# Optimization experiments

Measured on AMD Instinct MI355X. Metric: run time of the kernel, lower is better.

Reference implementation:

```python
import jax, jax.numpy as jnp
import numpy as np

NUM_GRAPHS = 256
EPS = 1e-5
SLOPE = 0.01

def _lrelu(x):
    return jnp.where(x >= 0, x, SLOPE * x)

def _gcn(x, W, b, src, dst, ew, n_nodes):
    # GCNConv(normalize=False): out[dst] = sum_e ew[e] * (x @ W)[src[e]] + b
    h = x @ W
    msg = h[src] * ew[:, None]
    agg = jax.ops.segment_sum(msg, dst, num_segments=n_nodes)
    return agg + b

def _bn(x, g, beta):
    # training-mode BatchNorm1d over node dim, biased variance
    m = jnp.mean(x, axis=0)
    v = jnp.mean((x - m) ** 2, axis=0)
    return (x - m) * jax.lax.rsqrt(v + EPS) * g + beta

def setup_inputs() -> dict:
    key = jax.random.key(0)
    ks = jax.random.split(key, 20)
    N, E, F0 = 20000, 320000, 1280
    dims = [(F0, 640), (640, 512), (512, 256), (256, 256)]
    inp = {
        'x': jax.random.normal(ks[0], (N, F0), dtype=jnp.float32),
        'edge_index': jax.random.randint(ks[1], (2, E), 0, N, dtype=jnp.int64),
        'edge_weigth': jax.random.uniform(ks[2], (E,), dtype=jnp.float32),
        'batch': jnp.sort(jax.random.randint(ks[3], (N,), 0, NUM_GRAPHS, dtype=jnp.int64)),
    }
    for i, (fi, fo) in enumerate(dims, start=1):
        inp[f'W{i}'] = jax.random.normal(ks[3 + i], (fi, fo), dtype=jnp.float32) * (1.0 / np.sqrt(fi))
        inp[f'b{i}'] = jnp.zeros((fo,), dtype=jnp.float32)
        inp[f'g{i}'] = jnp.ones((fo,), dtype=jnp.float32)
        inp[f'be{i}'] = jnp.zeros((fo,), dtype=jnp.float32)
    fdims = [(256, 128), (128, 64), (64, 2)]
    for i, (fi, fo) in enumerate(fdims, start=1):
        inp[f'Wf{i}'] = jax.random.normal(ks[10 + i], (fi, fo), dtype=jnp.float32) * np.sqrt(2.0 / (fi + fo))
        inp[f'bf{i}'] = jnp.zeros((fo,), dtype=jnp.float32)
    return inp

def reference(x, edge_index, edge_weigth, batch,
              W1, b1, g1, be1, W2, b2, g2, be2,
              W3, b3, g3, be3, W4, b4, g4, be4,
              Wf1, bf1, Wf2, bf2, Wf3, bf3):
    n = x.shape[0]
    src, dst = edge_index[0], edge_index[1]
    h = _lrelu(_bn(_gcn(x, W1, b1, src, dst, edge_weigth, n), g1, be1))
    h = _lrelu(_bn(_gcn(h, W2, b2, src, dst, edge_weigth, n), g2, be2))
    h = _lrelu(_bn(_gcn(h, W3, b3, src, dst, edge_weigth, n), g3, be3))
    h = _lrelu(_bn(_gcn(h, W4, b4, src, dst, edge_weigth, n), g4, be4))
    pooled = jax.ops.segment_sum(h, batch, num_segments=NUM_GRAPHS)  # [G, 256]
    out = _lrelu(pooled @ Wf1 + bf1)
    out = _lrelu(out @ Wf2 + bf2)
    out = _lrelu(out @ Wf3 + bf3)
    return out
```

## Files before the change

kernel.cpp:

```cpp
#include <hip/hip_runtime.h>

typedef short bf16x8 __attribute__((ext_vector_type(8)));
typedef float f32x4  __attribute__((ext_vector_type(4)));

__device__ __forceinline__ float bf2f(unsigned short h){
  union { unsigned int u; float f; } c; c.u = ((unsigned int)h) << 16; return c.f;
}
__device__ __forceinline__ unsigned short f2bf(float f){
  union { float f; unsigned int u; } c; c.f = f;
  unsigned int u = c.u;
  return (unsigned short)((u + 0x7fffu + ((u >> 16) & 1u)) >> 16);
}
__device__ __forceinline__ void gload_lds16(const void* g, void* l){
  __builtin_amdgcn_global_load_lds((const __attribute__((address_space(1))) unsigned int*)g,
                                   (__attribute__((address_space(3))) unsigned int*)l, 16, 0, 0);
}
__device__ __forceinline__ float lrelu(float x){ return x >= 0.f ? x : 0.01f * x; }

__global__ void cvt_f32_bf16(const float* __restrict__ x, unsigned short* __restrict__ o, int n4){
  int i = blockIdx.x * 256 + threadIdx.x;
  if (i >= n4) return;
  float4 v = ((const float4*)x)[i];
  ushort4 r; r.x = f2bf(v.x); r.y = f2bf(v.y); r.z = f2bf(v.z); r.w = f2bf(v.w);
  ((ushort4*)o)[i] = r;
}

__global__ void wt_kernel(const float* __restrict__ Wm, unsigned short* __restrict__ Wt, int K, int Nf){
  __shared__ float tile[32][33];
  int n0 = blockIdx.x * 32, k0 = blockIdx.y * 32;
  int tx = threadIdx.x, ty = threadIdx.y;
  for (int i = ty; i < 32; i += 8)
    tile[i][tx] = Wm[(size_t)(k0 + i) * Nf + n0 + tx];
  __syncthreads();
  for (int i = ty; i < 32; i += 8)
    Wt[(size_t)(n0 + i) * K + k0 + tx] = f2bf(tile[tx][i]);
}

__global__ void hist_kernel(const int* __restrict__ dst, int* __restrict__ hist, int E){
  int e = blockIdx.x * 256 + threadIdx.x;
  if (e < E) atomicAdd(&hist[dst[e]], 1);
}

__global__ void scan_kernel(int* __restrict__ hist, int* __restrict__ cursor, int n, int total){
  __shared__ int partials[1024];
  const int CH = 20;
  int t = threadIdx.x;
  int base = t * CH;
  int local[CH];
  int s = 0;
  for (int i = 0; i < CH; i++){
    int idx = base + i;
    int v = (idx < n) ? hist[idx] : 0;
    local[i] = s; s += v;
  }
  partials[t] = s;
  __syncthreads();
  for (int off = 1; off < 1024; off <<= 1){
    int v = (t >= off) ? partials[t - off] : 0;
    __syncthreads();
    if (t >= off) partials[t] += v;
    __syncthreads();
  }
  int pre = (t == 0) ? 0 : partials[t - 1];
  for (int i = 0; i < CH; i++){
    int idx = base + i;
    if (idx < n){ int v = pre + local[i]; hist[idx] = v; cursor[idx] = v; }
  }
  if (t == 0){ hist[n] = total; }
}

__global__ void scatter_kernel(const int* __restrict__ src, const int* __restrict__ dst,
                               const float* __restrict__ ew, int* __restrict__ cursor,
                               int* __restrict__ so, float* __restrict__ eo, int E){
  int e = blockIdx.x * 256 + threadIdx.x;
  if (e >= E) return;
  int d = dst[e];
  int p = atomicAdd(&cursor[d], 1);
  so[p] = src[e]; eo[p] = ew[e];
}

__global__ __launch_bounds__(256) void gemm_bf16(const unsigned short* __restrict__ A,
                                                 const unsigned short* __restrict__ Bt,
                                                 unsigned short* __restrict__ C,
                                                 int Nf, int K){
  __shared__ unsigned short lsA[128 * 64];
  __shared__ unsigned short lsB[128 * 64];
  const int tid = threadIdx.x;
  const int wave = tid >> 6, lane = tid & 63;
  const int wr = wave >> 1, wc = wave & 1;
  const size_t tm = (size_t)blockIdx.x * 128, tn = (size_t)blockIdx.y * 128;

  f32x4 acc[4][4] = {};

  const int lrow = lane >> 3;
  const int lcol = (lane & 7) * 8;
  const unsigned short* Ab = A  + (tm + wave * 32 + lrow) * (size_t)K + lcol;
  const unsigned short* Bb = Bt + (tn + wave * 32 + lrow) * (size_t)K + lcol;
  unsigned short* lA0 = &lsA[(wave * 32) * 64];
  unsigned short* lB0 = &lsB[(wave * 32) * 64];

  for (int k0 = 0; k0 < K; k0 += 64){
    #pragma unroll
    for (int s = 0; s < 4; s++){
      gload_lds16(Ab + (size_t)s * 8 * K + k0, lA0 + s * 8 * 64);
      gload_lds16(Bb + (size_t)s * 8 * K + k0, lB0 + s * 8 * 64);
    }
    __syncthreads();
    #pragma unroll
    for (int kk = 0; kk < 2; kk++){
      bf16x8 af[4], bfr[4];
      #pragma unroll
      for (int m = 0; m < 4; m++)
        af[m] = *(const bf16x8*)&lsA[(wr * 64 + m * 16 + (lane & 15)) * 64 + kk * 32 + (lane >> 4) * 8];
      #pragma unroll
      for (int n = 0; n < 4; n++)
        bfr[n] = *(const bf16x8*)&lsB[(wc * 64 + n * 16 + (lane & 15)) * 64 + kk * 32 + (lane >> 4) * 8];
      #pragma unroll
      for (int m = 0; m < 4; m++)
        #pragma unroll
        for (int n = 0; n < 4; n++)
          acc[m][n] = __builtin_amdgcn_mfma_f32_16x16x32_bf16(af[m], bfr[n], acc[m][n], 0, 0, 0);
    }
    __syncthreads();
  }
  #pragma unroll
  for (int m = 0; m < 4; m++)
    #pragma unroll
    for (int n = 0; n < 4; n++)
      #pragma unroll
      for (int j = 0; j < 4; j++){
        size_t row = tm + wr * 64 + m * 16 + (lane >> 4) * 4 + j;
        size_t col = tn + wc * 64 + n * 16 + (lane & 15);
        C[row * Nf + col] = f2bf(acc[m][n][j]);
      }
}

template<int F, int G>
__global__ __launch_bounds__((F / 8) * G)
void agg_csr_v(const unsigned short* __restrict__ H,
               const int* __restrict__ rp,
               const int* __restrict__ srcs,
               const float* __restrict__ ews,
               float* __restrict__ AGG){
  constexpr int CH = F / 8;
  const int node = blockIdx.x;
  const int t = threadIdx.x;
  const int c = t % CH, g = t / CH;
  const int e0 = rp[node], e1 = rp[node + 1];
  const size_t coff = (size_t)c * 8;

  float acc[8] = {0.f,0.f,0.f,0.f,0.f,0.f,0.f,0.f};
  int e = e0 + g;
  for (; e + G < e1; e += 2 * G){
    int s0 = srcs[e];     float w0 = ews[e];
    int s1 = srcs[e + G]; float w1 = ews[e + G];
    bf16x8 v0 = *(const bf16x8*)&H[(size_t)s0 * F + coff];
    bf16x8 v1 = *(const bf16x8*)&H[(size_t)s1 * F + coff];
    #pragma unroll
    for (int j = 0; j < 8; j++) acc[j] += w0 * bf2f((unsigned short)v0[j]);
    #pragma unroll
    for (int j = 0; j < 8; j++) acc[j] += w1 * bf2f((unsigned short)v1[j]);
  }
  if (e < e1){
    int s0 = srcs[e]; float w0 = ews[e];
    bf16x8 v0 = *(const bf16x8*)&H[(size_t)s0 * F + coff];
    #pragma unroll
    for (int j = 0; j < 8; j++) acc[j] += w0 * bf2f((unsigned short)v0[j]);
  }

  __shared__ float red[G][F];
  if (g > 0){
    #pragma unroll
    for (int j = 0; j < 8; j++) red[g][c * 8 + j] = acc[j];
  }
  __syncthreads();
  if (g == 0){
    #pragma unroll
    for (int gg = 1; gg < G; gg++)
      #pragma unroll
      for (int j = 0; j < 8; j++) acc[j] += red[gg][c * 8 + j];
    float* orow = AGG + (size_t)node * F + coff;
    #pragma unroll
    for (int j = 0; j < 8; j++) orow[j] = acc[j];
  }
}

__global__ void stats_kernel(const float* __restrict__ AGG, float* __restrict__ sum,
                             float* __restrict__ sumsq, int F){
  int f = blockIdx.x * 256 + threadIdx.x;
  if (f >= F) return;
  int r0 = blockIdx.y * 500;
  const float* p = AGG + (size_t)r0 * F + f;
  float s = 0.f, q = 0.f;
  for (int r = 0; r < 500; r++){ float v = p[(size_t)r * F]; s += v; q += v * v; }
  atomicAdd(&sum[f], s); atomicAdd(&sumsq[f], q);
}

__global__ void norm_kernel(const float* __restrict__ AGG, const float* __restrict__ sum,
                            const float* __restrict__ sumsq, const float* __restrict__ gw,
                            const float* __restrict__ bw, unsigned short* __restrict__ OUT, int F){
  int r = blockIdx.x;
  const float inv = 1.0f / 20000.0f;
  for (int f = threadIdx.x; f < F; f += 256){
    float m = sum[f] * inv;
    float v = fmaxf(sumsq[f] * inv - m * m, 0.f);
    float rs = rsqrtf(v + 1e-5f);
    float x = (AGG[(size_t)r * F + f] - m) * rs * gw[f] + bw[f];
    OUT[(size_t)r * F + f] = f2bf(lrelu(x));
  }
}

__global__ void bounds_kernel(const int* __restrict__ batch, int* __restrict__ gstart, int n){
  int g = threadIdx.x;
  if (g > 256) return;
  int lo = 0, hi = n;
  while (lo < hi){ int mid = (lo + hi) >> 1; if (batch[mid] < g) lo = mid + 1; else hi = mid; }
  gstart[g] = lo;
}

__global__ __launch_bounds__(256) void pool_kernel_v(const unsigned short* __restrict__ A1,
                                                     const int* __restrict__ gstart,
                                                     float* __restrict__ pooled){
  int gph = blockIdx.x;
  int t = threadIdx.x;
  int c = t & 31, g = t >> 5;
  int r0 = gstart[gph], r1 = gstart[gph + 1];
  float acc[8] = {0.f,0.f,0.f,0.f,0.f,0.f,0.f,0.f};
  for (int r = r0 + g; r < r1; r += 8){
    bf16x8 v = *(const bf16x8*)&A1[(size_t)r * 256 + c * 8];
    #pragma unroll
    for (int j = 0; j < 8; j++) acc[j] += bf2f((unsigned short)v[j]);
  }
  __shared__ float red[8][256];
  if (g > 0){
    #pragma unroll
    for (int j = 0; j < 8; j++) red[g][c * 8 + j] = acc[j];
  }
  __syncthreads();
  if (g == 0){
    #pragma unroll
    for (int gg = 1; gg < 8; gg++)
      #pragma unroll
      for (int j = 0; j < 8; j++) acc[j] += red[gg][c * 8 + j];
    #pragma unroll
    for (int j = 0; j < 8; j++) pooled[gph * 256 + c * 8 + j] = acc[j];
  }
}

__global__ void fc_kernel(const float* __restrict__ pooled,
                          const float* __restrict__ Wf1, const float* __restrict__ bf1,
                          const float* __restrict__ Wf2, const float* __restrict__ bf2,
                          const float* __restrict__ Wf3, const float* __restrict__ bf3,
                          float* __restrict__ out){
  int g = blockIdx.x, t = threadIdx.x;
  __shared__ float p0[256], p1[128], p2[64];
  p0[t] = pooled[g * 256 + t];
  p0[t + 128] = pooled[g * 256 + t + 128];
  __syncthreads();
  float a = bf1[t];
  for (int k = 0; k < 256; k++) a += p0[k] * Wf1[k * 128 + t];
  p1[t] = lrelu(a);
  __syncthreads();
  if (t < 64){
    float a2 = bf2[t];
    for (int k = 0; k < 128; k++) a2 += p1[k] * Wf2[k * 64 + t];
    p2[t] = lrelu(a2);
  }
  __syncthreads();
  if (t < 2){
    float a3 = bf3[t];
    for (int k = 0; k < 64; k++) a3 += p2[k] * Wf3[k * 2 + t];
    out[g * 2 + t] = lrelu(a3);
  }
}

extern "C" void kernel_launch(void* const* d_in, const int* in_sizes, int n_in,
                              void* d_out, int out_size, void* d_ws, size_t ws_size,
                              hipStream_t stream){
  const int N = 20000, E = 320000;
  const float* x     = (const float*)d_in[0];
  const int*   ei    = (const int*)d_in[1];
  const float* ew    = (const float*)d_in[2];
  const int*   batch = (const int*)d_in[3];
  const float* W[4]  = {(const float*)d_in[4], (const float*)d_in[8], (const float*)d_in[12], (const float*)d_in[16]};
  const float* gw[4] = {(const float*)d_in[6], (const float*)d_in[10], (const float*)d_in[14], (const float*)d_in[18]};
  const float* bw[4] = {(const float*)d_in[7], (const float*)d_in[11], (const float*)d_in[15], (const float*)d_in[19]};
  const float* Wf1 = (const float*)d_in[20]; const float* bf1 = (const float*)d_in[21];
  const float* Wf2 = (const float*)d_in[22]; const float* bf2 = (const float*)d_in[23];
  const float* Wf3 = (const float*)d_in[24]; const float* bf3 = (const float*)d_in[25];

  const int Kd[4] = {1280, 640, 512, 256};
  const int Nd[4] = {640, 512, 256, 256};

  char* w = (char*)d_ws;
  unsigned short* XB = (unsigned short*)w;
  float* AGG = (float*)w;                 w += 51445760;
  unsigned short* H  = (unsigned short*)w; w += 25722880;
  unsigned short* A1 = (unsigned short*)w; w += 25722880;
  unsigned short* WT = (unsigned short*)w; w += 1638400;
  int*   hist   = (int*)w;   w += 80128;
  int*   cursor = (int*)w;   w += 80128;
  int*   srcs   = (int*)w;   w += 1280000;
  float* ews    = (float*)w; w += 1280000;
  float* sum    = (float*)w; w += 2560;
  float* sumsq  = (float*)w; w += 2560;
  int*   gstart = (int*)w;   w += 1280;
  float* pooled = (float*)w; w += 262144;
  (void)ws_size; (void)n_in; (void)in_sizes; (void)out_size;

  cvt_f32_bf16<<<(N * 1280 / 4 + 255) / 256, 256, 0, stream>>>(x, XB, N * 1280 / 4);

  hipMemsetAsync(hist, 0, 80128, stream);
  hist_kernel<<<E / 256, 256, 0, stream>>>(ei + E, hist, E);
  scan_kernel<<<1, 1024, 0, stream>>>(hist, cursor, N, E);
  scatter_kernel<<<E / 256, 256, 0, stream>>>(ei, ei + E, ew, cursor, srcs, ews, E);

  bounds_kernel<<<1, 320, 0, stream>>>(batch, gstart, N);

  const unsigned short* in = XB;
  for (int l = 0; l < 4; l++){
    int K = Kd[l], Nf = Nd[l];
    wt_kernel<<<dim3(Nf / 32, K / 32), dim3(32, 8), 0, stream>>>(W[l], WT, K, Nf);
    gemm_bf16<<<dim3(157, Nf / 128), 256, 0, stream>>>(in, WT, H, Nf, K);
    if (Nf == 640)      agg_csr_v<640, 4><<<N, 320, 0, stream>>>(H, hist, srcs, ews, AGG);
    else if (Nf == 512) agg_csr_v<512, 4><<<N, 256, 0, stream>>>(H, hist, srcs, ews, AGG);
    else                agg_csr_v<256, 8><<<N, 256, 0, stream>>>(H, hist, srcs, ews, AGG);
    hipMemsetAsync(sum, 0, 5120, stream);
    stats_kernel<<<dim3((Nf + 255) / 256, 40), 256, 0, stream>>>(AGG, sum, sumsq, Nf);
    norm_kernel<<<N, 256, 0, stream>>>(AGG, sum, sumsq, gw[l], bw[l], A1, Nf);
    in = A1;
  }

  pool_kernel_v<<<256, 256, 0, stream>>>(A1, gstart, pooled);
  fc_kernel<<<256, 128, 0, stream>>>(pooled, Wf1, bf1, Wf2, bf2, Wf3, bf3, (float*)d_out);
}
```

Before: 777.2 us.

## Use 8-wave GEMM blocks with swapped grid order, vectorize BN stats and normalize

The bf16 GEMM now runs 512 threads (8 waves) per 128x128 tile, each wave owning a 32x64 sub-tile. The grid axes are swapped so blocks that share the same A rows launch next to each other. The BatchNorm statistics and normalize kernels now load and store float4 and ushort4 instead of scalars. The intent is better latency hiding and L2 reuse in the GEMM, and fewer memory transactions in the BN kernels. The trade-off is that the stats kernel now launches fewer threads (one per four features), which reduces its parallelism.

```diff
diff --git a/kernel.cpp b/kernel.cpp
--- a/kernel.cpp
+++ b/kernel.cpp
@@ -79,44 +79,43 @@
   so[p] = src[e]; eo[p] = ew[e];
 }
 
-__global__ __launch_bounds__(256) void gemm_bf16(const unsigned short* __restrict__ A,
-                                                 const unsigned short* __restrict__ Bt,
-                                                 unsigned short* __restrict__ C,
-                                                 int Nf, int K){
+__global__ __launch_bounds__(512) void gemm_bf16_8w(const unsigned short* __restrict__ A,
+                                                    const unsigned short* __restrict__ Bt,
+                                                    unsigned short* __restrict__ C,
+                                                    int Nf, int K){
   __shared__ unsigned short lsA[128 * 64];
   __shared__ unsigned short lsB[128 * 64];
   const int tid = threadIdx.x;
-  const int wave = tid >> 6, lane = tid & 63;
-  const int wr = wave >> 1, wc = wave & 1;
-  const size_t tm = (size_t)blockIdx.x * 128, tn = (size_t)blockIdx.y * 128;
-
-  f32x4 acc[4][4] = {};
-
-  const int lrow = lane >> 3;
-  const int lcol = (lane & 7) * 8;
-  const unsigned short* Ab = A  + (tm + wave * 32 + lrow) * (size_t)K + lcol;
-  const unsigned short* Bb = Bt + (tn + wave * 32 + lrow) * (size_t)K + lcol;
-  unsigned short* lA0 = &lsA[(wave * 32) * 64];
-  unsigned short* lB0 = &lsB[(wave * 32) * 64];
+  const int wv = tid >> 6, ln = tid & 63;
+  const int wr = wv >> 1, wc = wv & 1;
+  const size_t tn = (size_t)blockIdx.x * 128, tm = (size_t)blockIdx.y * 128;
+
+  f32x4 acc[2][4] = {};
+
+  const int srow = tid >> 3;
+  const int scol = (tid & 7) * 8;
+  const unsigned short* Ab = A  + (tm + srow) * (size_t)K + scol;
+  const unsigned short* Bb = Bt + (tn + srow) * (size_t)K + scol;
+  unsigned short* lA = lsA + tid * 8;
+  unsigned short* lB = lsB + tid * 8;
 
   for (int k0 = 0; k0 < K; k0 += 64){
-    #pragma unroll
-    for (int s = 0; s < 4; s++){
-      gload_lds16(Ab + (size_t)s * 8 * K + k0, lA0 + s * 8 * 64);
-      gload_lds16(Bb + (size_t)s * 8 * K + k0, lB0 + s * 8 * 64);
-    }
+    gload_lds16(Ab + k0, lA);
+    gload_lds16(Ab + (size_t)64 * K + k0, lA + 64 * 64);
+    gload_lds16(Bb + k0, lB);
+    gload_lds16(Bb + (size_t)64 * K + k0, lB + 64 * 64);
     __syncthreads();
     #pragma unroll
     for (int kk = 0; kk < 2; kk++){
-      bf16x8 af[4], bfr[4];
-      #pragma unroll
-      for (int m = 0; m < 4; m++)
-        af[m] = *(const bf16x8*)&lsA[(wr * 64 + m * 16 + (lane & 15)) * 64 + kk * 32 + (lane >> 4) * 8];
+      bf16x8 af[2], bfr[4];
+      #pragma unroll
+      for (int m = 0; m < 2; m++)
+        af[m] = *(const bf16x8*)&lsA[(wr * 32 + m * 16 + (ln & 15)) * 64 + kk * 32 + (ln >> 4) * 8];
       #pragma unroll
       for (int n = 0; n < 4; n++)
-        bfr[n] = *(const bf16x8*)&lsB[(wc * 64 + n * 16 + (lane & 15)) * 64 + kk * 32 + (lane >> 4) * 8];
-      #pragma unroll
-      for (int m = 0; m < 4; m++)
+        bfr[n] = *(const bf16x8*)&lsB[(wc * 64 + n * 16 + (ln & 15)) * 64 + kk * 32 + (ln >> 4) * 8];
+      #pragma unroll
+      for (int m = 0; m < 2; m++)
         #pragma unroll
         for (int n = 0; n < 4; n++)
           acc[m][n] = __builtin_amdgcn_mfma_f32_16x16x32_bf16(af[m], bfr[n], acc[m][n], 0, 0, 0);
@@ -124,13 +123,13 @@
     __syncthreads();
   }
   #pragma unroll
-  for (int m = 0; m < 4; m++)
+  for (int m = 0; m < 2; m++)
     #pragma unroll
     for (int n = 0; n < 4; n++)
       #pragma unroll
       for (int j = 0; j < 4; j++){
-        size_t row = tm + wr * 64 + m * 16 + (lane >> 4) * 4 + j;
-        size_t col = tn + wc * 64 + n * 16 + (lane & 15);
+        size_t row = tm + wr * 32 + m * 16 + (ln >> 4) * 4 + j;
+        size_t col = tn + wc * 64 + n * 16 + (ln & 15);
         C[row * Nf + col] = f2bf(acc[m][n][j]);
       }
 }
@@ -185,29 +184,55 @@
   }
 }
 
-__global__ void stats_kernel(const float* __restrict__ AGG, float* __restrict__ sum,
-                             float* __restrict__ sumsq, int F){
-  int f = blockIdx.x * 256 + threadIdx.x;
-  if (f >= F) return;
-  int r0 = blockIdx.y * 500;
-  const float* p = AGG + (size_t)r0 * F + f;
-  float s = 0.f, q = 0.f;
-  for (int r = 0; r < 500; r++){ float v = p[(size_t)r * F]; s += v; q += v * v; }
-  atomicAdd(&sum[f], s); atomicAdd(&sumsq[f], q);
-}
-
-__global__ void norm_kernel(const float* __restrict__ AGG, const float* __restrict__ sum,
-                            const float* __restrict__ sumsq, const float* __restrict__ gw,
-                            const float* __restrict__ bw, unsigned short* __restrict__ OUT, int F){
+__global__ void stats_kernel_v(const float* __restrict__ AGG, float* __restrict__ sum,
+                               float* __restrict__ sumsq, int F){
+  int nf4 = F >> 2;
+  int f4 = blockIdx.x * 256 + threadIdx.x;
+  if (f4 >= nf4) return;
+  const float4* p = (const float4*)(AGG + (size_t)blockIdx.y * 500 * F) + f4;
+  float4 s = {0.f,0.f,0.f,0.f}, q = {0.f,0.f,0.f,0.f};
+  for (int r = 0; r < 500; r++){
+    float4 v = p[(size_t)r * nf4];
+    s.x += v.x; s.y += v.y; s.z += v.z; s.w += v.w;
+    q.x += v.x*v.x; q.y += v.y*v.y; q.z += v.z*v.z; q.w += v.w*v.w;
+  }
+  atomicAdd(&sum[f4*4+0], s.x); atomicAdd(&sum[f4*4+1], s.y);
+  atomicAdd(&sum[f4*4+2], s.z); atomicAdd(&sum[f4*4+3], s.w);
+  atomicAdd(&sumsq[f4*4+0], q.x); atomicAdd(&sumsq[f4*4+1], q.y);
+  atomicAdd(&sumsq[f4*4+2], q.z); atomicAdd(&sumsq[f4*4+3], q.w);
+}
+
+__global__ void norm_kernel_v(const float* __restrict__ AGG, const float* __restrict__ sum,
+                              const float* __restrict__ sumsq, const float* __restrict__ gw,
+                              const float* __restrict__ bw, unsigned short* __restrict__ OUT, int F){
   int r = blockIdx.x;
+  int f4 = threadIdx.x;
+  int nf4 = F >> 2;
+  if (f4 >= nf4) return;
   const float inv = 1.0f / 20000.0f;
-  for (int f = threadIdx.x; f < F; f += 256){
-    float m = sum[f] * inv;
-    float v = fmaxf(sumsq[f] * inv - m * m, 0.f);
-    float rs = rsqrtf(v + 1e-5f);
-    float x = (AGG[(size_t)r * F + f] - m) * rs * gw[f] + bw[f];
-    OUT[(size_t)r * F + f] = f2bf(lrelu(x));
-  }
+  float4 s = ((const float4*)sum)[f4];
+  float4 q = ((const float4*)sumsq)[f4];
+  float4 g = ((const float4*)gw)[f4];
+  float4 b = ((const float4*)bw)[f4];
+  float4 a = ((const float4*)(AGG + (size_t)r * F))[f4];
+  ushort4 o;
+  {
+    float m = s.x * inv, v = fmaxf(q.x * inv - m * m, 0.f);
+    o.x = f2bf(lrelu((a.x - m) * rsqrtf(v + 1e-5f) * g.x + b.x));
+  }
+  {
+    float m = s.y * inv, v = fmaxf(q.y * inv - m * m, 0.f);
+    o.y = f2bf(lrelu((a.y - m) * rsqrtf(v + 1e-5f) * g.y + b.y));
+  }
+  {
+    float m = s.z * inv, v = fmaxf(q.z * inv - m * m, 0.f);
+    o.z = f2bf(lrelu((a.z - m) * rsqrtf(v + 1e-5f) * g.z + b.z));
+  }
+  {
+    float m = s.w * inv, v = fmaxf(q.w * inv - m * m, 0.f);
+    o.w = f2bf(lrelu((a.w - m) * rsqrtf(v + 1e-5f) * g.w + b.w));
+  }
+  ((ushort4*)(OUT + (size_t)r * F))[f4] = o;
 }
 
 __global__ void bounds_kernel(const int* __restrict__ batch, int* __restrict__ gstart, int n){
@@ -321,13 +346,13 @@
   for (int l = 0; l < 4; l++){
     int K = Kd[l], Nf = Nd[l];
     wt_kernel<<<dim3(Nf / 32, K / 32), dim3(32, 8), 0, stream>>>(W[l], WT, K, Nf);
-    gemm_bf16<<<dim3(157, Nf / 128), 256, 0, stream>>>(in, WT, H, Nf, K);
+    gemm_bf16_8w<<<dim3(Nf / 128, 157), 512, 0, stream>>>(in, WT, H, Nf, K);
     if (Nf == 640)      agg_csr_v<640, 4><<<N, 320, 0, stream>>>(H, hist, srcs, ews, AGG);
     else if (Nf == 512) agg_csr_v<512, 4><<<N, 256, 0, stream>>>(H, hist, srcs, ews, AGG);
     else                agg_csr_v<256, 8><<<N, 256, 0, stream>>>(H, hist, srcs, ews, AGG);
     hipMemsetAsync(sum, 0, 5120, stream);
-    stats_kernel<<<dim3((Nf + 255) / 256, 40), 256, 0, stream>>>(AGG, sum, sumsq, Nf);
-    norm_kernel<<<N, 256, 0, stream>>>(AGG, sum, sumsq, gw[l], bw[l], A1, Nf);
+    stats_kernel_v<<<dim3((Nf / 4 + 255) / 256, 40), 256, 0, stream>>>(AGG, sum, sumsq, Nf);
+    norm_kernel_v<<<N, 256, 0, stream>>>(AGG, sum, sumsq, gw[l], bw[l], A1, Nf);
     in = A1;
   }
 
```

After: 787.7 us. Within noise of the previous version (+1.4%).

## Remap GEMM blocks per XCD, panelize aggregation, vectorize BN stats and norm

Applied to the files above, without the earlier changes.

The GEMM grid is flattened and each block index is remapped so that consecutive tiles land on the same XCD, which should improve L2 reuse of A and B. Aggregation now splits the feature dimension into 8 panels and handles several nodes per block, with the panel index in the low bits of the block id so one XCD gathers from the same column slice and keeps it cache-resident. The stats and normalization kernels switch to float4 loads and stores, and normalization runs as a flat elementwise grid. The cost is more complex index math and a lower-occupancy 240-thread block for F=640.

```diff
diff --git a/kernel.cpp b/kernel.cpp
--- a/kernel.cpp
+++ b/kernel.cpp
@@ -82,13 +82,20 @@
 __global__ __launch_bounds__(256) void gemm_bf16(const unsigned short* __restrict__ A,
                                                  const unsigned short* __restrict__ Bt,
                                                  unsigned short* __restrict__ C,
-                                                 int Nf, int K){
+                                                 int Nf, int K, int Nt){
   __shared__ unsigned short lsA[128 * 64];
   __shared__ unsigned short lsB[128 * 64];
+  const int nwg = gridDim.x;
+  const int orig = blockIdx.x;
+  const int q = nwg >> 3, r = nwg & 7;
+  const int xcd = orig & 7, idx = orig >> 3;
+  const int wgid = (xcd < r ? xcd * (q + 1) : r * (q + 1) + (xcd - r) * q) + idx;
+  const int mt = wgid / Nt, nt = wgid % Nt;
+
   const int tid = threadIdx.x;
   const int wave = tid >> 6, lane = tid & 63;
   const int wr = wave >> 1, wc = wave & 1;
-  const size_t tm = (size_t)blockIdx.x * 128, tn = (size_t)blockIdx.y * 128;
+  const size_t tm = (size_t)mt * 128, tn = (size_t)nt * 128;
 
   f32x4 acc[4][4] = {};
 
@@ -135,19 +142,26 @@
       }
 }
 
-template<int F, int G>
-__global__ __launch_bounds__((F / 8) * G)
-void agg_csr_v(const unsigned short* __restrict__ H,
+template<int F, int C, int G, int NPB>
+__global__ __launch_bounds__(C * G * NPB)
+void agg_panel(const unsigned short* __restrict__ H,
                const int* __restrict__ rp,
                const int* __restrict__ srcs,
                const float* __restrict__ ews,
-               float* __restrict__ AGG){
-  constexpr int CH = F / 8;
-  const int node = blockIdx.x;
+               float* __restrict__ AGG, int Nnodes){
+  const int flat = blockIdx.x;
+  const int panel = flat & 7;
+  const int ngrp = flat >> 3;
   const int t = threadIdx.x;
-  const int c = t % CH, g = t / CH;
-  const int e0 = rp[node], e1 = rp[node + 1];
-  const size_t coff = (size_t)c * 8;
+  const int c = t % C;
+  const int g = (t / C) % G;
+  const int ni = t / (C * G);
+  const int node = ngrp * NPB + ni;
+  const bool valid = (node < Nnodes);
+  const size_t coff = (size_t)panel * (C * 8) + (size_t)c * 8;
+
+  int e0 = 0, e1 = 0;
+  if (valid){ e0 = rp[node]; e1 = rp[node + 1]; }
 
   float acc[8] = {0.f,0.f,0.f,0.f,0.f,0.f,0.f,0.f};
   int e = e0 + g;
@@ -168,46 +182,64 @@
     for (int j = 0; j < 8; j++) acc[j] += w0 * bf2f((unsigned short)v0[j]);
   }
 
-  __shared__ float red[G][F];
+  __shared__ float red[NPB * G * C * 8];
   if (g > 0){
     #pragma unroll
-    for (int j = 0; j < 8; j++) red[g][c * 8 + j] = acc[j];
-  }
-  __syncthreads();
-  if (g == 0){
+    for (int j = 0; j < 8; j++) red[((ni * G + g) * C + c) * 8 + j] = acc[j];
+  }
+  __syncthreads();
+  if (g == 0 && valid){
     #pragma unroll
     for (int gg = 1; gg < G; gg++)
       #pragma unroll
-      for (int j = 0; j < 8; j++) acc[j] += red[gg][c * 8 + j];
+      for (int j = 0; j < 8; j++) acc[j] += red[((ni * G + gg) * C + c) * 8 + j];
     float* orow = AGG + (size_t)node * F + coff;
-    #pragma unroll
-    for (int j = 0; j < 8; j++) orow[j] = acc[j];
-  }
-}
-
-__global__ void stats_kernel(const float* __restrict__ AGG, float* __restrict__ sum,
-                             float* __restrict__ sumsq, int F){
-  int f = blockIdx.x * 256 + threadIdx.x;
-  if (f >= F) return;
-  int r0 = blockIdx.y * 500;
-  const float* p = AGG + (size_t)r0 * F + f;
-  float s = 0.f, q = 0.f;
-  for (int r = 0; r < 500; r++){ float v = p[(size_t)r * F]; s += v; q += v * v; }
-  atomicAdd(&sum[f], s); atomicAdd(&sumsq[f], q);
-}
-
-__global__ void norm_kernel(const float* __restrict__ AGG, const float* __restrict__ sum,
-                            const float* __restrict__ sumsq, const float* __restrict__ gw,
-                            const float* __restrict__ bw, unsigned short* __restrict__ OUT, int F){
-  int r = blockIdx.x;
+    *(float4*)(orow)     = *(float4*)&acc[0];
+    *(float4*)(orow + 4) = *(float4*)&acc[4];
+  }
+}
+
+__global__ void stats_kernel_v(const float* __restrict__ AGG, float* __restrict__ sum,
+                               float* __restrict__ sumsq, int F){
+  int nf4 = F >> 2;
+  int f4 = blockIdx.x * 256 + threadIdx.x;
+  if (f4 >= nf4) return;
+  const float4* p = (const float4*)(AGG + (size_t)blockIdx.y * 500 * F) + f4;
+  float4 s = {0.f,0.f,0.f,0.f}, q = {0.f,0.f,0.f,0.f};
+  for (int r = 0; r < 500; r++){
+    float4 v = p[(size_t)r * nf4];
+    s.x += v.x; s.y += v.y; s.z += v.z; s.w += v.w;
+    q.x += v.x*v.x; q.y += v.y*v.y; q.z += v.z*v.z; q.w += v.w*v.w;
+  }
+  atomicAdd(&sum[f4*4+0], s.x); atomicAdd(&sum[f4*4+1], s.y);
+  atomicAdd(&sum[f4*4+2], s.z); atomicAdd(&sum[f4*4+3], s.w);
+  atomicAdd(&sumsq[f4*4+0], q.x); atomicAdd(&sumsq[f4*4+1], q.y);
+  atomicAdd(&sumsq[f4*4+2], q.z); atomicAdd(&sumsq[f4*4+3], q.w);
+}
+
+__global__ void norm_kernel_v2(const float* __restrict__ AGG, const float* __restrict__ sum,
+                               const float* __restrict__ sumsq, const float* __restrict__ gw,
+                               const float* __restrict__ bw, unsigned short* __restrict__ OUT,
+                               int nf4, int total4){
+  int i = blockIdx.x * 256 + threadIdx.x;
+  if (i >= total4) return;
+  int f4 = i % nf4;
   const float inv = 1.0f / 20000.0f;
-  for (int f = threadIdx.x; f < F; f += 256){
-    float m = sum[f] * inv;
-    float v = fmaxf(sumsq[f] * inv - m * m, 0.f);
-    float rs = rsqrtf(v + 1e-5f);
-    float x = (AGG[(size_t)r * F + f] - m) * rs * gw[f] + bw[f];
-    OUT[(size_t)r * F + f] = f2bf(lrelu(x));
-  }
+  float4 s = ((const float4*)sum)[f4];
+  float4 q = ((const float4*)sumsq)[f4];
+  float4 g = ((const float4*)gw)[f4];
+  float4 b = ((const float4*)bw)[f4];
+  float4 a = ((const float4*)AGG)[i];
+  ushort4 o;
+  { float m = s.x * inv, v = fmaxf(q.x * inv - m * m, 0.f);
+    o.x = f2bf(lrelu((a.x - m) * rsqrtf(v + 1e-5f) * g.x + b.x)); }
+  { float m = s.y * inv, v = fmaxf(q.y * inv - m * m, 0.f);
+    o.y = f2bf(lrelu((a.y - m) * rsqrtf(v + 1e-5f) * g.y + b.y)); }
+  { float m = s.z * inv, v = fmaxf(q.z * inv - m * m, 0.f);
+    o.z = f2bf(lrelu((a.z - m) * rsqrtf(v + 1e-5f) * g.z + b.z)); }
+  { float m = s.w * inv, v = fmaxf(q.w * inv - m * m, 0.f);
+    o.w = f2bf(lrelu((a.w - m) * rsqrtf(v + 1e-5f) * g.w + b.w)); }
+  ((ushort4*)OUT)[i] = o;
 }
 
 __global__ void bounds_kernel(const int* __restrict__ batch, int* __restrict__ gstart, int n){
@@ -320,14 +352,16 @@
   const unsigned short* in = XB;
   for (int l = 0; l < 4; l++){
     int K = Kd[l], Nf = Nd[l];
+    int Nt = Nf / 128;
     wt_kernel<<<dim3(Nf / 32, K / 32), dim3(32, 8), 0, stream>>>(W[l], WT, K, Nf);
-    gemm_bf16<<<dim3(157, Nf / 128), 256, 0, stream>>>(in, WT, H, Nf, K);
-    if (Nf == 640)      agg_csr_v<640, 4><<<N, 320, 0, stream>>>(H, hist, srcs, ews, AGG);
-    else if (Nf == 512) agg_csr_v<512, 4><<<N, 256, 0, stream>>>(H, hist, srcs, ews, AGG);
-    else                agg_csr_v<256, 8><<<N, 256, 0, stream>>>(H, hist, srcs, ews, AGG);
+    gemm_bf16<<<157 * Nt, 256, 0, stream>>>(in, WT, H, Nf, K, Nt);
+    if (Nf == 640)      agg_panel<640, 10, 8, 3><<<((N + 2) / 3) * 8, 240, 0, stream>>>(H, hist, srcs, ews, AGG, N);
+    else if (Nf == 512) agg_panel<512,  8, 8, 4><<<(N / 4) * 8, 256, 0, stream>>>(H, hist, srcs, ews, AGG, N);
+    else                agg_panel<256,  4, 8, 8><<<(N / 8) * 8, 256, 0, stream>>>(H, hist, srcs, ews, AGG, N);
     hipMemsetAsync(sum, 0, 5120, stream);
-    stats_kernel<<<dim3((Nf + 255) / 256, 40), 256, 0, stream>>>(AGG, sum, sumsq, Nf);
-    norm_kernel<<<N, 256, 0, stream>>>(AGG, sum, sumsq, gw[l], bw[l], A1, Nf);
+    stats_kernel_v<<<dim3((Nf / 4 + 255) / 256, 40), 256, 0, stream>>>(AGG, sum, sumsq, Nf);
+    int total4 = N * (Nf >> 2);
+    norm_kernel_v2<<<(total4 + 255) / 256, 256, 0, stream>>>(AGG, sum, sumsq, gw[l], bw[l], A1, Nf >> 2, total4);
     in = A1;
   }
 
```

New measurement: 815.3 us. 4.9% more time.
